# Kernel tuning notes

Hardware: AMD Instinct MI355X
Metric: run time of the kernel (lower is better)

Reference implementation:

```python
import jax, jax.numpy as jnp
import numpy as np


def setup_inputs() -> dict:
    key = jax.random.key(0)
    xyz = jax.random.normal(key, (16, 3, 4096), dtype=jnp.float32)  # (B,3,N), NCHW
    return {"xyz": xyz}


def _chamfer_means(a, b):
    # a: (B,N,3), b: (B,M,3); squared-distance chamfer, return per-batch means
    a2 = jnp.sum(a * a, axis=-1)            # (B,N)
    b2 = jnp.sum(b * b, axis=-1)            # (B,M)
    ab = jnp.einsum('bnd,bmd->bnm', a, b)   # (B,N,M)
    d2 = a2[:, :, None] + b2[:, None, :] - 2.0 * ab  # (B,N,M)
    dist12 = jnp.min(d2, axis=2)            # (B,N) nearest in b for each a
    dist21 = jnp.min(d2, axis=1)            # (B,M) nearest in a for each b
    return jnp.mean(dist12, axis=-1), jnp.mean(dist21, axis=-1)


def reference(xyz):
    # SymmetryLoss with sym_plane=('yz',): mirror x-coordinate (dim 0 of channel axis)
    mult = jnp.array([-1.0, 1.0, 1.0], dtype=xyz.dtype).reshape(1, 3, 1)
    m_xyz = jax.lax.stop_gradient(xyz * mult)   # mirrored points are detached
    a = jnp.transpose(m_xyz, (0, 2, 1))         # (B,N,3) generated (mirrored)
    b = jnp.transpose(xyz, (0, 2, 1))           # (B,N,3) reference
    mean12, mean21 = _chamfer_means(a, b)
    # LabeledChamferDistance with beta=0, gamma=1, delta=0:
    # loss = mean_b[ mean(dist12) + gamma * mean(dist21) ]
    loss = jnp.mean(mean12 + mean21)
    return loss
```

## Files before the change

kernel.cpp:

```cpp
#include <hip/hip_runtime.h>

#define BATCH 16
#define NPTS 4096
#define TOTN (BATCH * NPTS)
#define MH 8
#define MC (NPTS / MH)

typedef _Float16 f16;
typedef __attribute__((ext_vector_type(8))) _Float16 f16x8;
typedef __attribute__((ext_vector_type(16))) float f32x16;

__device__ __forceinline__ unsigned pk(f16 a, f16 b) {
    union { f16 h[2]; unsigned u; } t;
    t.h[0] = a; t.h[1] = b;
    return t.u;
}

__device__ __forceinline__ float min3f(float a, float b, float c) {
    return fminf(fminf(a, b), c);
}

__device__ __forceinline__ float treemin(const f32x16& d, float acc) {
    float t0 = min3f(d[0], d[1], d[2]);
    float t1 = min3f(d[3], d[4], d[5]);
    float t2 = min3f(d[6], d[7], d[8]);
    float t3 = min3f(d[9], d[10], d[11]);
    float t4 = min3f(d[12], d[13], d[14]);
    float u0 = min3f(t0, t1, t2);
    float u1 = min3f(t3, t4, d[15]);
    return min3f(acc, u0, u1);
}

__global__ __launch_bounds__(256, 4) void chamfer_mfma_kernel(
    const float* __restrict__ xyz, float* __restrict__ partials) {
    __shared__ uint4 T0[MC];
    __shared__ uint4 T1[MC];

    const int tid = threadIdx.x;
    const int lane = tid & 63;
    const int wid = tid >> 6;
    const int lm = lane & 31;
    const int kh = lane >> 5;

    const int mh = blockIdx.x & 7;
    const int nsup = (blockIdx.x >> 3) & 7;
    const int b = blockIdx.x >> 6;
    const float* base = xyz + (size_t)b * 3 * NPTS;

    const int m0 = mh * MC;
    for (int i = tid; i < MC; i += 256) {
        int mg = m0 + i;
        float x = base[mg], y = base[NPTS + mg], z = base[2 * NPTS + mg];
        float cx = -2.f * x, cy = -2.f * y, cz = -2.f * z;
        float b2 = fmaf(x, x, fmaf(y, y, z * z));
        f16 cxh = (f16)cx; f16 cxl = (f16)(cx - (float)cxh);
        f16 cyh = (f16)cy; f16 cyl = (f16)(cy - (float)cyh);
        f16 czh = (f16)cz; f16 czl = (f16)(cz - (float)czh);
        f16 b2h = (f16)b2; f16 b2l = (f16)(b2 - (float)b2h);
        T0[i] = make_uint4(pk(cxh, cxh), pk(cxl, cyh), pk(cyh, cyl), pk(czh, czh));
        T1[i] = make_uint4(pk(czl, b2h), pk(b2l, (f16)0.f), 0u, 0u);
    }
    __syncthreads();

    const int n0 = nsup * 512 + wid * 128;
    f16x8 Bf[4];
#pragma unroll
    for (int tile = 0; tile < 4; ++tile) {
        int n = n0 + tile * 32 + lm;
        float ax = -base[n];
        float ay = base[NPTS + n];
        float az = base[2 * NPTS + n];
        f16 axh = (f16)ax; f16 axl = (f16)(ax - (float)axh);
        f16 ayh = (f16)ay; f16 ayl = (f16)(ay - (float)ayh);
        f16 azh = (f16)az; f16 azl = (f16)(az - (float)azh);
        union { unsigned u[4]; f16x8 v; } B;
        if (kh == 0) {
            B.u[0] = pk(axh, axl); B.u[1] = pk(axh, ayh);
            B.u[2] = pk(ayl, ayh); B.u[3] = pk(azh, azl);
        } else {
            B.u[0] = pk(azh, (f16)1.f); B.u[1] = pk((f16)1.f, (f16)0.f);
            B.u[2] = 0u; B.u[3] = 0u;
        }
        Bf[tile] = B.v;
    }

    const uint4* Ab = kh ? T1 : T0;
    float acc0 = 1e30f, acc1 = 1e30f, acc2 = 1e30f, acc3 = 1e30f;
    const f32x16 zero = {};

#pragma unroll 2
    for (int t = 0; t < MC / 32; ++t) {
        union { uint4 q; f16x8 v; } A;
        A.q = Ab[t * 32 + lm];
        f32x16 d0 = __builtin_amdgcn_mfma_f32_32x32x16_f16(A.v, Bf[0], zero, 0, 0, 0);
        f32x16 d1 = __builtin_amdgcn_mfma_f32_32x32x16_f16(A.v, Bf[1], zero, 0, 0, 0);
        f32x16 d2 = __builtin_amdgcn_mfma_f32_32x32x16_f16(A.v, Bf[2], zero, 0, 0, 0);
        f32x16 d3 = __builtin_amdgcn_mfma_f32_32x32x16_f16(A.v, Bf[3], zero, 0, 0, 0);
        acc0 = treemin(d0, acc0);
        acc1 = treemin(d1, acc1);
        acc2 = treemin(d2, acc2);
        acc3 = treemin(d3, acc3);
    }

    acc0 = fminf(acc0, __shfl_xor(acc0, 32, 64));
    acc1 = fminf(acc1, __shfl_xor(acc1, 32, 64));
    acc2 = fminf(acc2, __shfl_xor(acc2, 32, 64));
    acc3 = fminf(acc3, __shfl_xor(acc3, 32, 64));

    if (lane < 32) {
        float* dst = partials + (size_t)mh * TOTN + b * NPTS + n0 + lm;
        dst[0] = acc0;
        dst[32] = acc1;
        dst[64] = acc2;
        dst[96] = acc3;
    }
}

__global__ __launch_bounds__(256) void combine_kernel(
    const float* __restrict__ xyz, const float* __restrict__ partials,
    float* __restrict__ blocksums) {
    __shared__ float red[4];
    const int n = blockIdx.x * 256 + threadIdx.x;
    float v = partials[n];
#pragma unroll
    for (int s = 1; s < MH; ++s) v = fminf(v, partials[(size_t)s * TOTN + n]);

    const int b = n >> 12;
    const int i = n & (NPTS - 1);
    const float* base = xyz + (size_t)b * 3 * NPTS;
    float x = base[i], y = base[NPTS + i], z = base[2 * NPTS + i];
    float sum = v + fmaf(x, x, fmaf(y, y, z * z));

#pragma unroll
    for (int off = 32; off; off >>= 1) sum += __shfl_down(sum, off, 64);
    if ((threadIdx.x & 63) == 0) red[threadIdx.x >> 6] = sum;
    __syncthreads();
    if (threadIdx.x == 0)
        blocksums[blockIdx.x] = (red[0] + red[1]) + (red[2] + red[3]);
}

__global__ __launch_bounds__(256) void final_kernel(
    const float* __restrict__ blocksums, float* __restrict__ out) {
    __shared__ float red[4];
    float v = blocksums[threadIdx.x];
#pragma unroll
    for (int off = 32; off; off >>= 1) v += __shfl_down(v, off, 64);
    if ((threadIdx.x & 63) == 0) red[threadIdx.x >> 6] = v;
    __syncthreads();
    if (threadIdx.x == 0)
        out[0] = ((red[0] + red[1]) + (red[2] + red[3])) * (2.0f / (float)TOTN);
}

extern "C" void kernel_launch(void* const* d_in, const int* in_sizes, int n_in,
                              void* d_out, int out_size, void* d_ws, size_t ws_size,
                              hipStream_t stream) {
    const float* xyz = (const float*)d_in[0];
    float* out = (float*)d_out;
    float* partials = (float*)d_ws;
    float* blocksums = partials + (size_t)MH * TOTN;

    chamfer_mfma_kernel<<<BATCH * 8 * MH, 256, 0, stream>>>(xyz, partials);
    combine_kernel<<<TOTN / 256, 256, 0, stream>>>(xyz, partials, blocksums);
    final_kernel<<<1, 256, 0, stream>>>(blocksums, out);
}
```

Baseline: 19.34 us.

## Switch chamfer distance tiles from 32x32x16 to 16x16x32 MFMA

Replaces the 32x32x16 f16 MFMA tiles with 16x16x32 tiles. The two K-halves of each M point's packed data are read from an interleaved LDS array, and lanes in the upper K quarters feed zeros. Each wave now covers 64 N points instead of 128, the grid doubles, and launch bounds ask for 6 blocks per CU. This aims to cut accumulator register pressure and the per-tile min-reduction depth, at the cost of half the K dimension doing zero work and more MFMA instructions per distance.

After: 33.29 us. +72.1%, slower.

```diff
diff --git a/kernel.cpp b/kernel.cpp
--- a/kernel.cpp
+++ b/kernel.cpp
@@ -8,7 +8,7 @@
 
 typedef _Float16 f16;
 typedef __attribute__((ext_vector_type(8))) _Float16 f16x8;
-typedef __attribute__((ext_vector_type(16))) float f32x16;
+typedef __attribute__((ext_vector_type(4))) float f32x4;
 
 __device__ __forceinline__ unsigned pk(f16 a, f16 b) {
     union { f16 h[2]; unsigned u; } t;
@@ -20,31 +20,19 @@
     return fminf(fminf(a, b), c);
 }
 
-__device__ __forceinline__ float treemin(const f32x16& d, float acc) {
-    float t0 = min3f(d[0], d[1], d[2]);
-    float t1 = min3f(d[3], d[4], d[5]);
-    float t2 = min3f(d[6], d[7], d[8]);
-    float t3 = min3f(d[9], d[10], d[11]);
-    float t4 = min3f(d[12], d[13], d[14]);
-    float u0 = min3f(t0, t1, t2);
-    float u1 = min3f(t3, t4, d[15]);
-    return min3f(acc, u0, u1);
-}
-
-__global__ __launch_bounds__(256, 4) void chamfer_mfma_kernel(
+__global__ __launch_bounds__(256, 6) void chamfer_mfma_kernel(
     const float* __restrict__ xyz, float* __restrict__ partials) {
-    __shared__ uint4 T0[MC];
-    __shared__ uint4 T1[MC];
+    __shared__ uint4 T[MC * 2];
 
     const int tid = threadIdx.x;
     const int lane = tid & 63;
     const int wid = tid >> 6;
-    const int lm = lane & 31;
-    const int kh = lane >> 5;
+    const int col = lane & 15;
+    const int kq = lane >> 4;
 
     const int mh = blockIdx.x & 7;
-    const int nsup = (blockIdx.x >> 3) & 7;
-    const int b = blockIdx.x >> 6;
+    const int nsup = (blockIdx.x >> 3) & 15;
+    const int b = blockIdx.x >> 7;
     const float* base = xyz + (size_t)b * 3 * NPTS;
 
     const int m0 = mh * MC;
@@ -53,66 +41,72 @@
         float x = base[mg], y = base[NPTS + mg], z = base[2 * NPTS + mg];
         float cx = -2.f * x, cy = -2.f * y, cz = -2.f * z;
         float b2 = fmaf(x, x, fmaf(y, y, z * z));
-        f16 cxh = (f16)cx; f16 cxl = (f16)(cx - (float)cxh);
-        f16 cyh = (f16)cy; f16 cyl = (f16)(cy - (float)cyh);
-        f16 czh = (f16)cz; f16 czl = (f16)(cz - (float)czh);
-        f16 b2h = (f16)b2; f16 b2l = (f16)(b2 - (float)b2h);
-        T0[i] = make_uint4(pk(cxh, cxh), pk(cxl, cyh), pk(cyh, cyl), pk(czh, czh));
-        T1[i] = make_uint4(pk(czl, b2h), pk(b2l, (f16)0.f), 0u, 0u);
+        f16 cxh = (f16)cx, cxl = (f16)(cx - (float)cxh);
+        f16 cyh = (f16)cy, cyl = (f16)(cy - (float)cyh);
+        f16 czh = (f16)cz, czl = (f16)(cz - (float)czh);
+        f16 b2h = (f16)b2, b2l = (f16)(b2 - (float)b2h);
+        T[i * 2 + 0] = make_uint4(pk(cxh, cxh), pk(cxl, cyh), pk(cyh, cyl), pk(czh, czh));
+        T[i * 2 + 1] = make_uint4(pk(czl, b2h), pk(b2l, (f16)0.f), 0u, 0u);
     }
     __syncthreads();
 
-    const int n0 = nsup * 512 + wid * 128;
+    const int n0 = nsup * 256 + wid * 64;
     f16x8 Bf[4];
 #pragma unroll
-    for (int tile = 0; tile < 4; ++tile) {
-        int n = n0 + tile * 32 + lm;
+    for (int j = 0; j < 4; ++j) {
+        int n = n0 + j * 16 + col;
         float ax = -base[n];
         float ay = base[NPTS + n];
         float az = base[2 * NPTS + n];
-        f16 axh = (f16)ax; f16 axl = (f16)(ax - (float)axh);
-        f16 ayh = (f16)ay; f16 ayl = (f16)(ay - (float)ayh);
-        f16 azh = (f16)az; f16 azl = (f16)(az - (float)azh);
+        f16 axh = (f16)ax, axl = (f16)(ax - (float)axh);
+        f16 ayh = (f16)ay, ayl = (f16)(ay - (float)ayh);
+        f16 azh = (f16)az, azl = (f16)(az - (float)azh);
         union { unsigned u[4]; f16x8 v; } B;
-        if (kh == 0) {
+        if (kq == 0) {
             B.u[0] = pk(axh, axl); B.u[1] = pk(axh, ayh);
             B.u[2] = pk(ayl, ayh); B.u[3] = pk(azh, azl);
-        } else {
+        } else if (kq == 1) {
             B.u[0] = pk(azh, (f16)1.f); B.u[1] = pk((f16)1.f, (f16)0.f);
             B.u[2] = 0u; B.u[3] = 0u;
+        } else {
+            B.u[0] = 0u; B.u[1] = 0u; B.u[2] = 0u; B.u[3] = 0u;
         }
-        Bf[tile] = B.v;
+        Bf[j] = B.v;
     }
 
-    const uint4* Ab = kh ? T1 : T0;
     float acc0 = 1e30f, acc1 = 1e30f, acc2 = 1e30f, acc3 = 1e30f;
-    const f32x16 zero = {};
+    const f32x4 zero = {};
+    const uint4 zq = make_uint4(0u, 0u, 0u, 0u);
 
 #pragma unroll 2
-    for (int t = 0; t < MC / 32; ++t) {
+    for (int t = 0; t < MC / 16; ++t) {
         union { uint4 q; f16x8 v; } A;
-        A.q = Ab[t * 32 + lm];
-        f32x16 d0 = __builtin_amdgcn_mfma_f32_32x32x16_f16(A.v, Bf[0], zero, 0, 0, 0);
-        f32x16 d1 = __builtin_amdgcn_mfma_f32_32x32x16_f16(A.v, Bf[1], zero, 0, 0, 0);
-        f32x16 d2 = __builtin_amdgcn_mfma_f32_32x32x16_f16(A.v, Bf[2], zero, 0, 0, 0);
-        f32x16 d3 = __builtin_amdgcn_mfma_f32_32x32x16_f16(A.v, Bf[3], zero, 0, 0, 0);
-        acc0 = treemin(d0, acc0);
-        acc1 = treemin(d1, acc1);
-        acc2 = treemin(d2, acc2);
-        acc3 = treemin(d3, acc3);
+        A.q = (kq < 2) ? T[(t * 16 + col) * 2 + kq] : zq;
+        f32x4 d0 = __builtin_amdgcn_mfma_f32_16x16x32_f16(A.v, Bf[0], zero, 0, 0, 0);
+        f32x4 d1 = __builtin_amdgcn_mfma_f32_16x16x32_f16(A.v, Bf[1], zero, 0, 0, 0);
+        f32x4 d2 = __builtin_amdgcn_mfma_f32_16x16x32_f16(A.v, Bf[2], zero, 0, 0, 0);
+        f32x4 d3 = __builtin_amdgcn_mfma_f32_16x16x32_f16(A.v, Bf[3], zero, 0, 0, 0);
+        acc0 = min3f(min3f(d0[0], d0[1], d0[2]), d0[3], acc0);
+        acc1 = min3f(min3f(d1[0], d1[1], d1[2]), d1[3], acc1);
+        acc2 = min3f(min3f(d2[0], d2[1], d2[2]), d2[3], acc2);
+        acc3 = min3f(min3f(d3[0], d3[1], d3[2]), d3[3], acc3);
     }
 
+    acc0 = fminf(acc0, __shfl_xor(acc0, 16, 64));
     acc0 = fminf(acc0, __shfl_xor(acc0, 32, 64));
+    acc1 = fminf(acc1, __shfl_xor(acc1, 16, 64));
     acc1 = fminf(acc1, __shfl_xor(acc1, 32, 64));
+    acc2 = fminf(acc2, __shfl_xor(acc2, 16, 64));
     acc2 = fminf(acc2, __shfl_xor(acc2, 32, 64));
+    acc3 = fminf(acc3, __shfl_xor(acc3, 16, 64));
     acc3 = fminf(acc3, __shfl_xor(acc3, 32, 64));
 
-    if (lane < 32) {
-        float* dst = partials + (size_t)mh * TOTN + b * NPTS + n0 + lm;
-        dst[0] = acc0;
-        dst[32] = acc1;
-        dst[64] = acc2;
-        dst[96] = acc3;
+    if (lane < 16) {
+        float* dst = partials + (size_t)mh * TOTN + b * NPTS + n0;
+        dst[col] = acc0;
+        dst[16 + col] = acc1;
+        dst[32 + col] = acc2;
+        dst[48 + col] = acc3;
     }
 }
 
@@ -159,7 +153,7 @@
     float* partials = (float*)d_ws;
     float* blocksums = partials + (size_t)MH * TOTN;
 
-    chamfer_mfma_kernel<<<BATCH * 8 * MH, 256, 0, stream>>>(xyz, partials);
+    chamfer_mfma_kernel<<<BATCH * 16 * MH, 256, 0, stream>>>(xyz, partials);
     combine_kernel<<<TOTN / 256, 256, 0, stream>>>(xyz, partials, blocksums);
     final_kernel<<<1, 256, 0, stream>>>(blocksums, out);
 }
```
